# Performance work log

Measured on AMD Instinct MI355X. Metric: run time of the kernel, lower is better.

Reference implementation:

```python
import jax, jax.numpy as jnp
import numpy as np

B, L, H = 2, 2048, 1024
NH, DK, DV = 4, 256, 256
CONV_K, FIR_S, FIR_L = 4, 3, 63
GATE_IN = H + 4 * 2 * NH  # 1056
MLP_H = 2 * H
CHUNK = 32


def l2norm(x):
    return x * jax.lax.rsqrt(jnp.sum(x * x, -1, keepdims=True) + 1e-6)


def causal_dwconv(x, w):
    # x: [b, l, c], w: [c, k]; causal depthwise cross-correlation == F.conv1d(pad left k-1, groups=c)
    k = w.shape[-1]
    xc = jnp.pad(jnp.transpose(x, (0, 2, 1)), ((0, 0), (0, 0), (k - 1, 0)))
    y = jax.lax.conv_general_dilated(xc, w[:, None, :], (1,), 'VALID',
                                     feature_group_count=w.shape[0],
                                     dimension_numbers=('NCH', 'OIH', 'NCH'))
    return jnp.transpose(y, (0, 2, 1))


def delta_rule_chunkwise(q, k, v, beta, chunk=CHUNK):
    # q,k: [b,h,L,dk]; v: [b,h,L,dv]; beta: [b,h,L]; L divisible by chunk
    b, h, Lp, dk = q.shape
    dv = v.shape[-1]
    n = Lp // chunk
    q = l2norm(q)
    k = l2norm(k)
    v = v * beta[..., None]
    kb = k * beta[..., None]
    qc, kc, vc, kbc = (t.reshape(b, h, n, chunk, -1) for t in (q, k, v, kb))
    # strictly-lower Gram matrix; the original in-place row loop computes inv(I + tril(kb k^T, -1))
    A = jnp.tril(jnp.einsum('bhnid,bhnjd->bhnij', kbc, kc), -1)
    T = jnp.linalg.inv(jnp.eye(chunk, dtype=q.dtype) + A)  # [b,h,n,c,c]
    u = T @ vc   # [b,h,n,c,dv]
    w = T @ kbc  # [b,h,n,c,dk]

    def step(S, inp):
        qi, ki, ui, wi = inp  # each [b,h,c,d]
        attn = jnp.tril(qi @ jnp.swapaxes(ki, -1, -2))  # keep diag (masked_fill triu(.,1))
        u2 = ui - wi @ S
        oi = qi @ S + attn @ u2
        return S + jnp.swapaxes(ki, -1, -2) @ u2, oi

    S0 = jnp.zeros((b, h, dk, dv), q.dtype)
    xs = tuple(jnp.moveaxis(t, 2, 0) for t in (qc, kc, u, w))
    S, o = jax.lax.scan(step, S0, xs)
    o = jnp.moveaxis(o, 0, 2).reshape(b, h, Lp, dv)
    return o, S


def branch_stats(x):
    # x: [b,l,h,d] -> [b,l,2h]  (mean and population-std, std clamped at sqrt(1e-6))
    m = x.mean(-1)
    s = jnp.sqrt(jnp.maximum(x.var(-1), 1e-6))
    return jnp.concatenate([m, s], -1)


def setup_inputs() -> dict:
    key = jax.random.key(0)
    ks = jax.random.split(key, 16)
    f32 = jnp.float32

    def dirac(k_, shape):
        f = 0.01 * jax.random.normal(k_, shape, f32)
        return f.at[..., shape[-1] // 2].add(1.0)

    b2 = jnp.zeros((NH * 4,), f32).at[jnp.arange(NH) * 4 + 3].set(2.0)
    return {
        'hidden_states': jax.random.normal(ks[0], (B, L, H), f32),
        'Wq': 0.02 * jax.random.normal(ks[1], (H, NH * DK), f32),
        'Wk': 0.02 * jax.random.normal(ks[2], (H, NH * DK), f32),
        'Wv': 0.02 * jax.random.normal(ks[3], (H, NH * DV), f32),
        'Wb': 0.02 * jax.random.normal(ks[4], (H, NH), f32),
        'conv_q_w': 0.2 * jax.random.normal(ks[5], (NH * DK, CONV_K), f32),
        'conv_k_w': 0.2 * jax.random.normal(ks[6], (NH * DK, CONV_K), f32),
        'conv_v_w': 0.2 * jax.random.normal(ks[7], (NH * DV, CONV_K), f32),
        'fir_short_w': dirac(ks[8], (NH, DV, FIR_S)),
        'fir_long_w': dirac(ks[9], (NH, DV, FIR_L)),
        'mlp_w1': 0.02 * jax.random.normal(ks[10], (GATE_IN, MLP_H), f32),
        'mlp_b1': jnp.zeros((MLP_H,), f32),
        'mlp_w2': 0.02 * jax.random.normal(ks[11], (MLP_H, NH * 4), f32),
        'mlp_b2': b2,
        'gate_log_temp': jnp.full((NH,), np.log(1.2), f32),
        'o_norm_w': jnp.ones((DV,), f32),
        'Wo': 0.02 * jax.random.normal(ks[12], (NH * DV, H), f32),
    }


def reference(hidden_states, Wq, Wk, Wv, Wb, conv_q_w, conv_k_w, conv_v_w,
              fir_short_w, fir_long_w, mlp_w1, mlp_b1, mlp_w2, mlp_b2,
              gate_log_temp, o_norm_w, Wo):
    x = hidden_states
    b, l, _ = x.shape
    # projections + short causal depthwise convs with silu (qk_activation='silu')
    q = jax.nn.silu(causal_dwconv(x @ Wq, conv_q_w)).reshape(b, l, NH, DK)
    k = jax.nn.silu(causal_dwconv(x @ Wk, conv_k_w)).reshape(b, l, NH, DK)
    v = jax.nn.silu(causal_dwconv(x @ Wv, conv_v_w)).reshape(b, l, NH, DV)
    beta = jax.nn.sigmoid(x @ Wb)  # [b,l,h]

    delta_out, _S = delta_rule_chunkwise(
        jnp.transpose(q, (0, 2, 1, 3)), jnp.transpose(k, (0, 2, 1, 3)),
        jnp.transpose(v, (0, 2, 1, 3)), jnp.transpose(beta, (0, 2, 1)))
    delta_out = jnp.transpose(delta_out, (0, 2, 1, 3))  # [b,l,h,dv]

    vf = v.reshape(b, l, NH * DV)
    fir_short = causal_dwconv(vf, fir_short_w.reshape(NH * DV, FIR_S)).reshape(b, l, NH, DV)
    fir_long = causal_dwconv(vf, fir_long_w.reshape(NH * DV, FIR_L)).reshape(b, l, NH, DV)

    gate_in = jnp.concatenate([x, branch_stats(fir_short), branch_stats(fir_long),
                               branch_stats(delta_out), branch_stats(v)], -1)
    logits = jax.nn.gelu(gate_in @ mlp_w1 + mlp_b1, approximate=False) @ mlp_w2 + mlp_b2
    temp = jax.nn.softplus(gate_log_temp) + 1e-4
    logits = logits.reshape(b, l, NH, 4) / temp[None, None, :, None]
    w = jax.nn.softmax(logits, -1)

    o = (w[..., 0:1] * fir_short + w[..., 1:2] * fir_long
         + w[..., 2:3] * delta_out + w[..., 3:4] * v)
    # RMSNorm over head_v_dim, eps=1e-5
    o = o * jax.lax.rsqrt(jnp.mean(o * o, -1, keepdims=True) + 1e-5) * o_norm_w
    return o.reshape(b, l, NH * DV) @ Wo
```

## Files before the change

kernel.cpp:

```cpp
#include <hip/hip_runtime.h>
#include <hip/hip_bf16.h>


#define DEVI __device__ __forceinline__
typedef unsigned int u32;
typedef unsigned short ushort_t;
typedef __attribute__((ext_vector_type(8))) short short8;
typedef __attribute__((ext_vector_type(4))) float floatx4;

constexpr int Ls = 2048, NH = 4;
constexpr int NCh = 64;

constexpr size_t off_xq   = 0;
constexpr size_t off_xk   = 4194304;
constexpr size_t off_xv   = 8388608;
constexpr size_t off_q    = 12582912;
constexpr size_t off_k    = 16777216;
constexpr size_t off_v    = 20971520;
constexpr size_t off_beta = 25165824;
constexpr size_t off_attn = 25182208;
constexpr size_t off_firs = 25706496;
constexpr size_t off_firl = 29900800;
constexpr size_t off_gin  = 34095104;
constexpr size_t off_mlph = 38420480;
constexpr size_t off_gates= 46809088;

DEVI float sigmoidf_(float x) { return 1.f / (1.f + expf(-x)); }
DEVI float siluf_(float x) { return x / (1.f + expf(-x)); }
DEVI float geluf_(float x) { return 0.5f * x * (1.f + erff(x * 0.7071067811865476f)); }
DEVI ushort_t f2bf(float f) {
  union { float f; u32 u; } c{f};
  u32 r = (c.u + 0x7fffu + ((c.u >> 16) & 1u)) >> 16;
  return (ushort_t)r;
}
DEVI float bf2f(ushort_t h) {
  union { u32 u; float f; } c; c.u = ((u32)h) << 16; return c.f;
}
DEVI void cvt8(float4 a, float4 b, short8& hi, short8& lo) {
  float f[8] = {a.x,a.y,a.z,a.w,b.x,b.y,b.z,b.w};
#pragma unroll
  for (int j = 0; j < 8; ++j) {
    ushort_t h = f2bf(f[j]);
    hi[j] = (short)h;
    lo[j] = (short)f2bf(f[j] - bf2f(h));
  }
}
DEVI void async16(const void* g, void* l) {
  __builtin_amdgcn_global_load_lds(
      (const u32 __attribute__((address_space(1)))*)g,
      (u32 __attribute__((address_space(3)))*)l, 16, 0, 0);
}

__global__ __launch_bounds__(256) void to_bf16(
    const float* __restrict__ in, ushort_t* __restrict__ out, int n)
{
  int i = (blockIdx.x * 256 + threadIdx.x) * 8;
  if (i >= n) return;
  float4 a = *(const float4*)(in + i);
  float4 b = *(const float4*)(in + i + 4);
  ushort_t o[8] = { f2bf(a.x), f2bf(a.y), f2bf(a.z), f2bf(a.w),
                    f2bf(b.x), f2bf(b.y), f2bf(b.z), f2bf(b.w) };
  *(uint4*)(out + i) = *(uint4*)o;
}

__global__ __launch_bounds__(256) void convT(
    const float* __restrict__ W, ushort_t* __restrict__ out, int Kq, int Nq)
{
  __shared__ ushort_t tile[32][33];
  int n0 = blockIdx.x * 32, k0 = blockIdx.y * 32;
  int tx = threadIdx.x & 31, ty = threadIdx.x >> 5;
#pragma unroll
  for (int r = 0; r < 32; r += 8)
    tile[ty + r][tx] = f2bf(W[(size_t)(k0 + ty + r) * Nq + n0 + tx]);
  __syncthreads();
#pragma unroll
  for (int r = 0; r < 32; r += 8)
    out[(size_t)(n0 + ty + r) * Kq + k0 + tx] = tile[tx][ty + r];
}

__global__ __launch_bounds__(256) void gemm_bf16(
    const ushort_t* __restrict__ A, const ushort_t* __restrict__ Bt,
    float* __restrict__ C, int Nq, int Kq,
    const float* __restrict__ bias, int act, int outbf)
{
  __shared__ ushort_t As[128 * 32];
  __shared__ ushort_t Bs[128 * 32];
  int t = threadIdx.x;
  int w = t >> 6, lane = t & 63;
  int m0 = blockIdx.y * 128, n0 = blockIdx.x * 128;
  floatx4 acc[4][4];
#pragma unroll
  for (int i = 0; i < 4; ++i)
#pragma unroll
    for (int j = 0; j < 4; ++j)
#pragma unroll
      for (int r = 0; r < 4; ++r) acc[i][j][r] = 0.f;

  int lrow = lane >> 2, lk8 = (lane & 3) * 8;
  for (int kt = 0; kt < Kq; kt += 32) {
#pragma unroll
    for (int r = 0; r < 2; ++r) {
      int seg = w * 2 + r;
      int row = seg * 16 + lrow;
      async16(A  + (size_t)(m0 + row) * Kq + kt + lk8, &As[seg * 512]);
      async16(Bt + (size_t)(n0 + row) * Kq + kt + lk8, &Bs[seg * 512]);
    }
    __syncthreads();
    short8 af[4], bf[4];
#pragma unroll
    for (int i = 0; i < 4; ++i) {
      int row = (w >> 1) * 64 + i * 16 + (lane & 15);
      af[i] = *(const short8*)&As[row * 32 + (lane >> 4) * 8];
    }
#pragma unroll
    for (int j = 0; j < 4; ++j) {
      int col = (w & 1) * 64 + j * 16 + (lane & 15);
      bf[j] = *(const short8*)&Bs[col * 32 + (lane >> 4) * 8];
    }
#pragma unroll
    for (int i = 0; i < 4; ++i)
#pragma unroll
      for (int j = 0; j < 4; ++j)
        acc[i][j] = __builtin_amdgcn_mfma_f32_16x16x32_bf16(af[i], bf[j], acc[i][j], 0, 0, 0);
    __syncthreads();
  }
#pragma unroll
  for (int i = 0; i < 4; ++i) {
    int rbase = m0 + (w >> 1) * 64 + i * 16 + ((lane >> 4) << 2);
#pragma unroll
    for (int j = 0; j < 4; ++j) {
      int col = n0 + (w & 1) * 64 + j * 16 + (lane & 15);
      float bv = act ? bias[col] : 0.f;
#pragma unroll
      for (int r = 0; r < 4; ++r) {
        float v = acc[i][j][r];
        if (act) v = geluf_(v + bv);
        if (outbf) ((ushort_t*)C)[(size_t)(rbase + r) * Nq + col] = f2bf(v);
        else       C[(size_t)(rbase + r) * Nq + col] = v;
      }
    }
  }
}

__global__ __launch_bounds__(256) void beta_sigmoid(
    const float* __restrict__ x, const float* __restrict__ Wb,
    float* __restrict__ beta)
{
  int mtok = blockIdx.x, t = threadIdx.x;
  int b = mtok >> 11, l = mtok & 2047;
  float a0 = 0, a1 = 0, a2 = 0, a3 = 0;
  for (int k = t; k < 1024; k += 256) {
    float xv = x[(size_t)mtok * 1024 + k];
    float4 w4 = *(const float4*)(Wb + k * 4);
    a0 = fmaf(xv, w4.x, a0); a1 = fmaf(xv, w4.y, a1);
    a2 = fmaf(xv, w4.z, a2); a3 = fmaf(xv, w4.w, a3);
  }
#pragma unroll
  for (int off = 32; off; off >>= 1) {
    a0 += __shfl_down(a0, off); a1 += __shfl_down(a1, off);
    a2 += __shfl_down(a2, off); a3 += __shfl_down(a3, off);
  }
  __shared__ float red[4][4];
  int w = t >> 6;
  if ((t & 63) == 0) { red[w][0] = a0; red[w][1] = a1; red[w][2] = a2; red[w][3] = a3; }
  __syncthreads();
  if (t < 4) {
    float s = red[0][t] + red[1][t] + red[2][t] + red[3][t];
    beta[((size_t)(b * NH + t)) * Ls + l] = sigmoidf_(s);
  }
}

__global__ __launch_bounds__(256) void conv_prep(
    const float* __restrict__ x3, const float* __restrict__ wq,
    const float* __restrict__ wk, const float* __restrict__ wv,
    const float* __restrict__ beta_g,
    float* __restrict__ qn, float* __restrict__ kn,
    float* __restrict__ kb, float* __restrict__ vb,
    float* __restrict__ v_out)
{
  int i = blockIdx.x;
  int t = threadIdx.x;
  int l = i & 2047, bh = i >> 11;
  int b = bh >> 2, h = bh & 3;
  int c = h * 256 + t;
  const float* p = x3 + ((size_t)b * Ls) * 3072 + c;
  float4 wq4 = *(const float4*)(wq + c * 4);
  float4 wk4 = *(const float4*)(wk + c * 4);
  float4 wv4 = *(const float4*)(wv + c * 4);
  float qw[4] = {wq4.x, wq4.y, wq4.z, wq4.w};
  float kw[4] = {wk4.x, wk4.y, wk4.z, wk4.w};
  float vw[4] = {wv4.x, wv4.y, wv4.z, wv4.w};
  float aq = 0.f, ak = 0.f, av = 0.f;
#pragma unroll
  for (int j = 0; j < 4; ++j) {
    int ls = l - 3 + j;
    if (ls >= 0) {
      size_t rb = (size_t)ls * 3072;
      aq = fmaf(qw[j], p[rb], aq);
      ak = fmaf(kw[j], p[rb + 1024], ak);
      av = fmaf(vw[j], p[rb + 2048], av);
    }
  }
  float qv = siluf_(aq), kv = siluf_(ak), vv = siluf_(av);
  float sq = qv * qv, sk = kv * kv;
#pragma unroll
  for (int off = 32; off; off >>= 1) {
    sq += __shfl_down(sq, off);
    sk += __shfl_down(sk, off);
  }
  __shared__ float rq_[4], rk_[4];
  int w = t >> 6;
  if ((t & 63) == 0) { rq_[w] = sq; rk_[w] = sk; }
  __syncthreads();
  sq = rq_[0] + rq_[1] + rq_[2] + rq_[3];
  sk = rk_[0] + rk_[1] + rk_[2] + rk_[3];
  float rq = rsqrtf(sq + 1e-6f), rk = rsqrtf(sk + 1e-6f);
  float bt = beta_g[i];
  size_t base = (size_t)i * 256 + t;
  qn[base] = qv * rq;
  kn[base] = kv * rk;
  kb[base] = kv * rk * bt;
  vb[base] = vv * bt;
  v_out[base] = vv;
}

__global__ __launch_bounds__(256) void chunk_prep(
    const float* __restrict__ kb, const float* __restrict__ kn,
    const float* __restrict__ qn, const float* __restrict__ vb,
    float* __restrict__ attn_g, float* __restrict__ u_out,
    ushort_t* __restrict__ wn_bf, ushort_t* __restrict__ q_bf,
    ushort_t* __restrict__ knT_bf)
{
  __shared__ float Am[32][33];
  __shared__ float Tm[32][36];
  __shared__ ushort_t KT_hi[256][40];
  __shared__ ushort_t KT_lo[256][40];
  int t = threadIdx.x;
  int cc = blockIdx.x & 63, bh = blockIdx.x >> 6;
  size_t gbase = ((size_t)bh * Ls + cc * 32) * 256;
  int wv = t >> 6, lane = t & 63;
  int l16 = lane & 15, quad = lane >> 4;
  int mi = wv >> 1, ni = wv & 1;

  floatx4 Aacc = {0.f,0.f,0.f,0.f}, Qacc = {0.f,0.f,0.f,0.f};
  {
    int mrow = mi * 16 + l16, nrow = ni * 16 + l16;
    const float* kbp = kb + gbase + (size_t)mrow * 256;
    const float* qnp = qn + gbase + (size_t)mrow * 256;
    const float* knp = kn + gbase + (size_t)nrow * 256;
#pragma unroll
    for (int ks = 0; ks < 8; ++ks) {
      int koff = ks * 32 + quad * 8;
      short8 kbh, kbl, qnh, qnl, knh, knl;
      cvt8(*(const float4*)(kbp + koff), *(const float4*)(kbp + koff + 4), kbh, kbl);
      cvt8(*(const float4*)(qnp + koff), *(const float4*)(qnp + koff + 4), qnh, qnl);
      cvt8(*(const float4*)(knp + koff), *(const float4*)(knp + koff + 4), knh, knl);
      Aacc = __builtin_amdgcn_mfma_f32_16x16x32_bf16(kbh, knh, Aacc, 0, 0, 0);
      Aacc = __builtin_amdgcn_mfma_f32_16x16x32_bf16(kbh, knl, Aacc, 0, 0, 0);
      Aacc = __builtin_amdgcn_mfma_f32_16x16x32_bf16(kbl, knh, Aacc, 0, 0, 0);
      Qacc = __builtin_amdgcn_mfma_f32_16x16x32_bf16(qnh, knh, Qacc, 0, 0, 0);
      Qacc = __builtin_amdgcn_mfma_f32_16x16x32_bf16(qnh, knl, Qacc, 0, 0, 0);
      Qacc = __builtin_amdgcn_mfma_f32_16x16x32_bf16(qnl, knh, Qacc, 0, 0, 0);
      if (ni == 0)
        *(uint4*)(q_bf + gbase + (size_t)mrow * 256 + koff) = *(uint4*)&qnh;
    }
  }
  float* ag = attn_g + ((size_t)bh * 64 + cc) * 1024;
#pragma unroll
  for (int r = 0; r < 4; ++r) {
    int row = mi * 16 + quad * 4 + r, col = ni * 16 + l16;
    Am[row][col] = (col < row) ? Aacc[r] : 0.f;
    ag[row * 32 + col] = (col <= row) ? Qacc[r] : 0.f;
  }
  __syncthreads();

  if (wv == 0) {
    if (t < 32) {
#pragma unroll
      for (int i = 0; i < 32; ++i) Tm[i][t] = (i == t) ? 1.f : 0.f;
      for (int i2 = 1; i2 < 32; ++i2) {
        if (t < i2) {
          float s = 0.f;
          for (int m2 = t; m2 < i2; ++m2) s = fmaf(Am[i2][m2], Tm[m2][t], s);
          Tm[i2][t] = -s;
        }
      }
    }
  } else {
    int base = t - 64;
#pragma unroll
    for (int pass = 0; pass < 2; ++pass) {
      int d = base + pass * 192;
      if (d < 256) {
        u32 hp[16], lp[16], kp2[16];
#pragma unroll
        for (int m2 = 0; m2 < 16; ++m2) {
          float f0 = kb[gbase + (size_t)(2 * m2) * 256 + d];
          float f1 = kb[gbase + (size_t)(2 * m2 + 1) * 256 + d];
          ushort_t h0 = f2bf(f0), h1 = f2bf(f1);
          hp[m2] = (u32)h0 | ((u32)h1 << 16);
          lp[m2] = (u32)f2bf(f0 - bf2f(h0)) | ((u32)f2bf(f1 - bf2f(h1)) << 16);
          float g0 = kn[gbase + (size_t)(2 * m2) * 256 + d];
          float g1 = kn[gbase + (size_t)(2 * m2 + 1) * 256 + d];
          kp2[m2] = (u32)f2bf(g0) | ((u32)f2bf(g1) << 16);
        }
#pragma unroll
        for (int q2 = 0; q2 < 4; ++q2) {
          *(uint4*)&KT_hi[d][q2 * 8] = *(uint4*)&hp[q2 * 4];
          *(uint4*)&KT_lo[d][q2 * 8] = *(uint4*)&lp[q2 * 4];
          *(uint4*)(knT_bf + gbase + (size_t)d * 32 + q2 * 8) = *(uint4*)&kp2[q2 * 4];
        }
      }
    }
  }
  __syncthreads();

  int lt = wv & 1, dgrp = wv >> 1;
  short8 Th, Tl;
  {
    int lrow = lt * 16 + l16;
    cvt8(*(const float4*)&Tm[lrow][quad * 8],
         *(const float4*)&Tm[lrow][quad * 8 + 4], Th, Tl);
  }
#pragma unroll
  for (int j = 0; j < 8; ++j) {
    int dt = dgrp * 8 + j;
    short8 Bh = *(const short8*)&KT_hi[dt * 16 + l16][quad * 8];
    short8 Bl = *(const short8*)&KT_lo[dt * 16 + l16][quad * 8];
    floatx4 acc = {0.f,0.f,0.f,0.f};
    acc = __builtin_amdgcn_mfma_f32_16x16x32_bf16(Th, Bh, acc, 0, 0, 0);
    acc = __builtin_amdgcn_mfma_f32_16x16x32_bf16(Th, Bl, acc, 0, 0, 0);
    acc = __builtin_amdgcn_mfma_f32_16x16x32_bf16(Tl, Bh, acc, 0, 0, 0);
#pragma unroll
    for (int r = 0; r < 4; ++r) {
      int row = lt * 16 + quad * 4 + r;
      wn_bf[gbase + (size_t)row * 256 + dt * 16 + l16] = f2bf(-acc[r]);
    }
  }
  __syncthreads();

  {
    int d = t;
    u32 hp[16], lp[16];
#pragma unroll
    for (int m2 = 0; m2 < 16; ++m2) {
      float f0 = vb[gbase + (size_t)(2 * m2) * 256 + d];
      float f1 = vb[gbase + (size_t)(2 * m2 + 1) * 256 + d];
      ushort_t h0 = f2bf(f0), h1 = f2bf(f1);
      hp[m2] = (u32)h0 | ((u32)h1 << 16);
      lp[m2] = (u32)f2bf(f0 - bf2f(h0)) | ((u32)f2bf(f1 - bf2f(h1)) << 16);
    }
#pragma unroll
    for (int q2 = 0; q2 < 4; ++q2) {
      *(uint4*)&KT_hi[d][q2 * 8] = *(uint4*)&hp[q2 * 4];
      *(uint4*)&KT_lo[d][q2 * 8] = *(uint4*)&lp[q2 * 4];
    }
  }
  __syncthreads();

#pragma unroll
  for (int j = 0; j < 8; ++j) {
    int dt = dgrp * 8 + j;
    short8 Bh = *(const short8*)&KT_hi[dt * 16 + l16][quad * 8];
    short8 Bl = *(const short8*)&KT_lo[dt * 16 + l16][quad * 8];
    floatx4 acc = {0.f,0.f,0.f,0.f};
    acc = __builtin_amdgcn_mfma_f32_16x16x32_bf16(Th, Bh, acc, 0, 0, 0);
    acc = __builtin_amdgcn_mfma_f32_16x16x32_bf16(Th, Bl, acc, 0, 0, 0);
    acc = __builtin_amdgcn_mfma_f32_16x16x32_bf16(Tl, Bh, acc, 0, 0, 0);
#pragma unroll
    for (int r = 0; r < 4; ++r) {
      int row = lt * 16 + quad * 4 + r;
      u_out[gbase + (size_t)row * 256 + dt * 16 + l16] = acc[r];
    }
  }
}

__global__ __launch_bounds__(256, 1) void delta_fir(
    const ushort_t* __restrict__ wn_bf, const ushort_t* __restrict__ q_bf,
    const ushort_t* __restrict__ knT_bf, const float* __restrict__ attn_g,
    const float* __restrict__ u_g, float* __restrict__ delta_g,
    const float* __restrict__ v, const float* __restrict__ wlg,
    const float* __restrict__ wsg, float* __restrict__ firl,
    float* __restrict__ firs)
{
  __shared__ __attribute__((aligned(16))) char smem[72704];
  int t = threadIdx.x;

  if (blockIdx.x >= 128) {
    float (*vt)[71] = (float(*)[71])smem;
    int bid = blockIdx.x - 128;
    int lt = bid & 255;
    int bh = bid >> 8;
    int b = bh >> 2, h = bh & 3;
    int l0 = lt * 8;
    const float* vp = v + (size_t)bh * Ls * 256;
    for (int r = 0; r < 70; ++r) {
      int ls = l0 - 62 + r;
      vt[t][r] = (ls >= 0) ? vp[(size_t)ls * 256 + t] : 0.f;
    }
    float TL[63], TS3[3];
#pragma unroll
    for (int j = 0; j < 63; ++j) TL[j] = wlg[((size_t)h * 256 + t) * 63 + j];
#pragma unroll
    for (int j = 0; j < 3; ++j) TS3[j] = wsg[((size_t)h * 256 + t) * 3 + j];
    __syncthreads();
    float aL[8] = {0,0,0,0,0,0,0,0}, aS[8] = {0,0,0,0,0,0,0,0};
#pragma unroll
    for (int r = 0; r < 70; ++r) {
      float vm = vt[t][r];
#pragma unroll
      for (int p = 0; p < 8; ++p) {
        int jl = r - p;
        if (jl >= 0 && jl < 63) aL[p] = fmaf(vm, TL[jl], aL[p]);
        int jssrc = r - 60 - p;
        if (jssrc >= 0 && jssrc < 3) aS[p] = fmaf(vm, TS3[jssrc], aS[p]);
      }
    }
#pragma unroll
    for (int p = 0; p < 8; ++p) {
      int l = l0 + p;
      size_t ob = (((size_t)b * Ls + l) * NH + h) * 256 + t;
      firl[ob] = aL[p];
      firs[ob] = aS[p];
    }
    return;
  }

  ushort_t (*Shi)[264] = (ushort_t(*)[264])(smem);
  ushort_t (*Slo)[264] = (ushort_t(*)[264])(smem + 8448);
  float (*u2L)[17] = (float(*)[17])(smem + 16896);
  int bh = blockIdx.x & 7, g = blockIdx.x >> 3;
  int b = bh >> 2, h = bh & 3;
  int wv = t >> 6, lane = t & 63;
  int lquad = lane >> 4, l16 = lane & 15;
  int j0 = g * 16;
  const ushort_t* wp = wn_bf + (size_t)bh * Ls * 256;
  const ushort_t* qp = q_bf  + (size_t)bh * Ls * 256;
  const ushort_t* kp = knT_bf + (size_t)bh * Ls * 256;
  const float* up = u_g + (size_t)bh * Ls * 256;
  const float* atp = attn_g + (size_t)bh * 64 * 1024;
  int Mt = wv & 1;
  bool isU = (wv < 2);
  floatx4 Sacc[4], SaccL[4];
#pragma unroll
  for (int i = 0; i < 4; ++i)
#pragma unroll
    for (int r = 0; r < 4; ++r) { Sacc[i][r] = 0.f; SaccL[i][r] = 0.f; }
  for (int i = t; i < 4224; i += 256) ((u32*)smem)[i] = 0;
  __syncthreads();
  const ushort_t* ap = (isU ? wp : qp) + (size_t)(Mt * 16 + l16) * 256;
  const ushort_t* kr = kp + (size_t)l16 * 32 + lquad * 8;
  const float* urow = up + (size_t)(Mt * 16 + lquad * 4) * 256 + j0 + l16;
  const float* arp = atp + (size_t)(Mt * 16 + l16) * 32 + lquad * 8;

  short8 aC[8], kC[4];
  floatx4 uC = {0.f, 0.f, 0.f, 0.f};
  float4 atC0 = {0,0,0,0}, atC1 = {0,0,0,0};
#pragma unroll
  for (int ks = 0; ks < 8; ++ks)
    aC[ks] = *(const short8*)(ap + ks * 32 + lquad * 8);
#pragma unroll
  for (int i = 0; i < 4; ++i)
    kC[i] = *(const short8*)(kr + (size_t)(wv * 4 + i) * 512);
  if (isU) {
#pragma unroll
    for (int r = 0; r < 4; ++r) uC[r] = urow[(size_t)r * 256];
  } else {
    atC0 = *(const float4*)(arp);
    atC1 = *(const float4*)(arp + 4);
  }

  for (int cc = 0; cc < NCh; ++cc) {
    size_t cb = (size_t)cc * 8192;
    short8 aN[8], kN[4];
    floatx4 uN = {0.f, 0.f, 0.f, 0.f};
    float4 atN0 = {0,0,0,0}, atN1 = {0,0,0,0};
    bool hasN = (cc + 1 < NCh);
    if (hasN) {
      size_t nb = cb + 8192;
#pragma unroll
      for (int ks = 0; ks < 8; ++ks)
        aN[ks] = *(const short8*)(ap + nb + ks * 32 + lquad * 8);
#pragma unroll
      for (int i = 0; i < 4; ++i)
        kN[i] = *(const short8*)(kr + nb + (size_t)(wv * 4 + i) * 512);
      if (isU) {
#pragma unroll
        for (int r = 0; r < 4; ++r) uN[r] = urow[nb + (size_t)r * 256];
      } else {
        size_t na = (size_t)(cc + 1) * 1024;
        atN0 = *(const float4*)(arp + na);
        atN1 = *(const float4*)(arp + na + 4);
      }
    }
    short8 ath, atl;
    if (!isU) cvt8(atC0, atC1, ath, atl);

    floatx4 acc;
    if (isU) {
      floatx4 a0 = uC, a1 = {0,0,0,0}, a2 = {0,0,0,0}, a3 = {0,0,0,0};
#pragma unroll
      for (int ks = 0; ks < 8; ++ks) {
        short8 sh = *(const short8*)&Shi[l16][ks * 32 + lquad * 8];
        short8 sl = *(const short8*)&Slo[l16][ks * 32 + lquad * 8];
        if (ks & 1) {
          a1 = __builtin_amdgcn_mfma_f32_16x16x32_bf16(aC[ks], sh, a1, 0, 0, 0);
          a3 = __builtin_amdgcn_mfma_f32_16x16x32_bf16(aC[ks], sl, a3, 0, 0, 0);
        } else {
          a0 = __builtin_amdgcn_mfma_f32_16x16x32_bf16(aC[ks], sh, a0, 0, 0, 0);
          a2 = __builtin_amdgcn_mfma_f32_16x16x32_bf16(aC[ks], sl, a2, 0, 0, 0);
        }
      }
#pragma unroll
      for (int r = 0; r < 4; ++r) acc[r] = (a0[r] + a1[r]) + (a2[r] + a3[r]);
#pragma unroll
      for (int r = 0; r < 4; ++r)
        u2L[Mt * 16 + lquad * 4 + r][l16] = acc[r];
    } else {
      floatx4 a0 = {0,0,0,0}, a1 = {0,0,0,0};
#pragma unroll
      for (int ks = 0; ks < 8; ++ks) {
        short8 sh = *(const short8*)&Shi[l16][ks * 32 + lquad * 8];
        if (ks & 1) a1 = __builtin_amdgcn_mfma_f32_16x16x32_bf16(aC[ks], sh, a1, 0, 0, 0);
        else        a0 = __builtin_amdgcn_mfma_f32_16x16x32_bf16(aC[ks], sh, a0, 0, 0, 0);
      }
#pragma unroll
      for (int r = 0; r < 4; ++r) acc[r] = a0[r] + a1[r];
    }
    __syncthreads();
    short8 uh, ul;
#pragma unroll
    for (int j = 0; j < 8; ++j) {
      float f = u2L[lquad * 8 + j][l16];
      ushort_t hi = f2bf(f);
      uh[j] = (short)hi;
      ul[j] = (short)f2bf(f - bf2f(hi));
    }
    if (!isU) {
      acc = __builtin_amdgcn_mfma_f32_16x16x32_bf16(ath, uh, acc, 0, 0, 0);
      acc = __builtin_amdgcn_mfma_f32_16x16x32_bf16(ath, ul, acc, 0, 0, 0);
      acc = __builtin_amdgcn_mfma_f32_16x16x32_bf16(atl, uh, acc, 0, 0, 0);
#pragma unroll
      for (int r = 0; r < 4; ++r) {
        int l = cc * 32 + Mt * 16 + lquad * 4 + r;
        delta_g[(((size_t)b * Ls + l) * NH + h) * 256 + j0 + l16] = acc[r];
      }
    }
#pragma unroll
    for (int i = 0; i < 4; ++i) {
      Sacc[i]  = __builtin_amdgcn_mfma_f32_16x16x32_bf16(kC[i], uh, Sacc[i], 0, 0, 0);
      SaccL[i] = __builtin_amdgcn_mfma_f32_16x16x32_bf16(kC[i], ul, SaccL[i], 0, 0, 0);
    }
#pragma unroll
    for (int i = 0; i < 4; ++i) {
      int dk0 = (wv * 4 + i) * 16 + lquad * 4;
      ushort4 h4, l4;
      ushort_t* hp = (ushort_t*)&h4;
      ushort_t* lp = (ushort_t*)&l4;
#pragma unroll
      for (int r = 0; r < 4; ++r) {
        float sv = Sacc[i][r] + SaccL[i][r];
        ushort_t hi = f2bf(sv);
        hp[r] = hi;
        lp[r] = f2bf(sv - bf2f(hi));
      }
      *(ushort4*)&Shi[l16][dk0] = h4;
      *(ushort4*)&Slo[l16][dk0] = l4;
    }
    __syncthreads();
    if (hasN) {
#pragma unroll
      for (int ks = 0; ks < 8; ++ks) aC[ks] = aN[ks];
#pragma unroll
      for (int i = 0; i < 4; ++i) kC[i] = kN[i];
      uC = uN;
      atC0 = atN0; atC1 = atN1;
    }
  }
}

__global__ __launch_bounds__(256) void build_gate_in_bf(
    const float* __restrict__ x, const float* __restrict__ firs,
    const float* __restrict__ firl, const float* __restrict__ delta,
    const float* __restrict__ v, ushort_t* __restrict__ gin)
{
  int mtok = blockIdx.x, t = threadIdx.x;
  int b = mtok >> 11, l = mtok & 2047;
  float4 xv = *(const float4*)(x + (size_t)mtok * 1024 + t * 4);
  ushort4 xo = make_ushort4(f2bf(xv.x), f2bf(xv.y), f2bf(xv.z), f2bf(xv.w));
  *(ushort4*)(gin + (size_t)mtok * 1056 + t * 4) = xo;
  int w = t >> 6, lane = t & 63;
  for (int br = 0; br < 4; ++br) {
    float s = 0.f, s2 = 0.f;
#pragma unroll
    for (int r = 0; r < 4; ++r) {
      int d = lane + r * 64;
      float val;
      if (br == 0)      val = firs [(size_t)mtok * 1024 + w * 256 + d];
      else if (br == 1) val = firl [(size_t)mtok * 1024 + w * 256 + d];
      else if (br == 2) val = delta[(size_t)mtok * 1024 + w * 256 + d];
      else              val = v[(((size_t)(b * NH + w)) * Ls + l) * 256 + d];
      s += val; s2 = fmaf(val, val, s2);
    }
#pragma unroll
    for (int off = 32; off; off >>= 1) {
      s += __shfl_down(s, off);
      s2 += __shfl_down(s2, off);
    }
    if (lane == 0) {
      float mean = s * (1.f / 256.f);
      float var = s2 * (1.f / 256.f) - mean * mean;
      gin[(size_t)mtok * 1056 + 1024 + br * 8 + w] = f2bf(mean);
      gin[(size_t)mtok * 1056 + 1024 + br * 8 + 4 + w] = f2bf(sqrtf(fmaxf(var, 1e-6f)));
    }
  }
}

__global__ __launch_bounds__(256) void mlp2_gates(
    const ushort_t* __restrict__ mh, const float* __restrict__ W2,
    const float* __restrict__ b2, const float* __restrict__ glt,
    float* __restrict__ gates)
{
  int mtok = blockIdx.x, t = threadIdx.x;
  float p[16];
#pragma unroll
  for (int j = 0; j < 16; ++j) p[j] = 0.f;
  for (int k = t; k < 2048; k += 256) {
    float hv = bf2f(mh[(size_t)mtok * 2048 + k]);
    const float* wr = W2 + (size_t)k * 16;
#pragma unroll
    for (int j4 = 0; j4 < 4; ++j4) {
      float4 w4 = *(const float4*)(wr + j4 * 4);
      p[j4*4+0] = fmaf(hv, w4.x, p[j4*4+0]);
      p[j4*4+1] = fmaf(hv, w4.y, p[j4*4+1]);
      p[j4*4+2] = fmaf(hv, w4.z, p[j4*4+2]);
      p[j4*4+3] = fmaf(hv, w4.w, p[j4*4+3]);
    }
  }
#pragma unroll
  for (int j = 0; j < 16; ++j)
#pragma unroll
    for (int off = 32; off; off >>= 1) p[j] += __shfl_down(p[j], off);
  __shared__ float red[4][16];
  __shared__ float zl[16];
  int w = t >> 6;
  if ((t & 63) == 0) {
#pragma unroll
    for (int j = 0; j < 16; ++j) red[w][j] = p[j];
  }
  __syncthreads();
  if (t < 16) {
    float tot = red[0][t] + red[1][t] + red[2][t] + red[3][t] + b2[t];
    float tempv = log1pf(expf(glt[t >> 2])) + 1e-4f;
    zl[t] = tot / tempv;
  }
  __syncthreads();
  if (t < 4) {
    float z0 = zl[t*4], z1 = zl[t*4+1], z2 = zl[t*4+2], z3 = zl[t*4+3];
    float mx = fmaxf(fmaxf(z0, z1), fmaxf(z2, z3));
    float e0 = expf(z0 - mx), e1 = expf(z1 - mx), e2 = expf(z2 - mx), e3 = expf(z3 - mx);
    float inv = 1.f / (e0 + e1 + e2 + e3);
    gates[(size_t)mtok * 16 + t * 4 + 0] = e0 * inv;
    gates[(size_t)mtok * 16 + t * 4 + 1] = e1 * inv;
    gates[(size_t)mtok * 16 + t * 4 + 2] = e2 * inv;
    gates[(size_t)mtok * 16 + t * 4 + 3] = e3 * inv;
  }
}

__global__ __launch_bounds__(256) void combine_norm_bf(
    const float* __restrict__ firs, const float* __restrict__ firl,
    const float* __restrict__ delta, const float* __restrict__ v,
    const float* __restrict__ gates, const float* __restrict__ onw,
    ushort_t* __restrict__ o)
{
  int mh = blockIdx.x;
  int mtok = mh >> 2, h = mh & 3;
  int t = threadIdx.x;
  int b = mtok >> 11, l = mtok & 2047;
  const float* g = gates + (size_t)mtok * 16 + h * 4;
  float w0 = g[0], w1 = g[1], w2 = g[2], w3 = g[3];
  size_t tb = (size_t)mtok * 1024 + h * 256 + t;
  float val = w0 * firs[tb] + w1 * firl[tb] + w2 * delta[tb]
            + w3 * v[(((size_t)(b * NH + h)) * Ls + l) * 256 + t];
  float s2 = val * val;
#pragma unroll
  for (int off = 32; off; off >>= 1) s2 += __shfl_down(s2, off);
  __shared__ float r4[4];
  if ((t & 63) == 0) r4[t >> 6] = s2;
  __syncthreads();
  float tot = r4[0] + r4[1] + r4[2] + r4[3];
  float rms = rsqrtf(tot * (1.f / 256.f) + 1e-5f);
  o[tb] = f2bf(val * rms * onw[t]);
}

extern "C" void kernel_launch(void* const* d_in, const int* in_sizes, int n_in,
                              void* d_out, int out_size, void* d_ws, size_t ws_size,
                              hipStream_t stream) {
  const float* x     = (const float*)d_in[0];
  const float* Wq    = (const float*)d_in[1];
  const float* Wk    = (const float*)d_in[2];
  const float* Wv    = (const float*)d_in[3];
  const float* Wb    = (const float*)d_in[4];
  const float* convq = (const float*)d_in[5];
  const float* convk = (const float*)d_in[6];
  const float* convv = (const float*)d_in[7];
  const float* firsw = (const float*)d_in[8];
  const float* firlw = (const float*)d_in[9];
  const float* mlpw1 = (const float*)d_in[10];
  const float* mlpb1 = (const float*)d_in[11];
  const float* mlpw2 = (const float*)d_in[12];
  const float* mlpb2 = (const float*)d_in[13];
  const float* glt   = (const float*)d_in[14];
  const float* onw   = (const float*)d_in[15];
  const float* Wo    = (const float*)d_in[16];
  float* ws = (float*)d_ws;

  ushort_t* x_bf   = (ushort_t*)(ws + off_firs);
  ushort_t* Wqkv_t = (ushort_t*)(ws + off_firl);
  ushort_t* gin_bf = (ushort_t*)(ws + off_gin);
  ushort_t* w1_t   = (ushort_t*)(ws + off_k);
  ushort_t* o_bf   = (ushort_t*)(ws + off_xv);
  ushort_t* Wo_t   = (ushort_t*)(ws + off_beta);
  ushort_t* mlph_bf= (ushort_t*)(ws + off_mlph);
  ushort_t* wn_bf  = (ushort_t*)(ws + off_firs);
  ushort_t* q_bf   = (ushort_t*)(ws + off_firs + 2097152);
  ushort_t* knT_bf = (ushort_t*)(ws + off_firl);
  float* x3   = ws + off_xq;
  float* kb_f = ws + off_gin;
  float* vb_f = ws + off_mlph;
  float* firs_f = ws + off_xq;
  float* firl_f = ws + off_xk;

  dim3 blk(256);
  to_bf16<<<2048, blk, 0, stream>>>(x, x_bf, 4194304);
  convT<<<dim3(32, 32), blk, 0, stream>>>(Wq, Wqkv_t, 1024, 1024);
  convT<<<dim3(32, 32), blk, 0, stream>>>(Wk, Wqkv_t + 1048576, 1024, 1024);
  convT<<<dim3(32, 32), blk, 0, stream>>>(Wv, Wqkv_t + 2097152, 1024, 1024);
  gemm_bf16<<<dim3(24, 32), blk, 0, stream>>>(x_bf, Wqkv_t, x3, 3072, 1024, nullptr, 0, 0);
  beta_sigmoid<<<4096, blk, 0, stream>>>(x, Wb, ws + off_beta);
  conv_prep<<<16384, blk, 0, stream>>>(x3, convq, convk, convv, ws + off_beta,
                                       ws + off_q, ws + off_k, kb_f, vb_f, ws + off_v);
  chunk_prep<<<512, blk, 0, stream>>>(kb_f, ws + off_k, ws + off_q, vb_f,
                                      ws + off_attn, ws + off_xv, wn_bf, q_bf, knT_bf);
  delta_fir<<<2176, blk, 0, stream>>>(wn_bf, q_bf, knT_bf, ws + off_attn,
                                      ws + off_xv, ws + off_q,
                                      ws + off_v, firlw, firsw, firl_f, firs_f);
  build_gate_in_bf<<<4096, blk, 0, stream>>>(x, firs_f, firl_f, ws + off_q,
                                             ws + off_v, gin_bf);
  convT<<<dim3(64, 33), blk, 0, stream>>>(mlpw1, w1_t, 1056, 2048);
  gemm_bf16<<<dim3(16, 32), blk, 0, stream>>>(gin_bf, w1_t, (float*)mlph_bf,
                                              2048, 1056, mlpb1, 1, 1);
  mlp2_gates<<<4096, blk, 0, stream>>>(mlph_bf, mlpw2, mlpb2, glt, ws + off_gates);
  combine_norm_bf<<<16384, blk, 0, stream>>>(firs_f, firl_f, ws + off_q,
                                             ws + off_v, ws + off_gates, onw, o_bf);
  convT<<<dim3(32, 32), blk, 0, stream>>>(Wo, Wo_t, 1024, 1024);
  gemm_bf16<<<dim3(8, 32), blk, 0, stream>>>(o_bf, Wo_t, (float*)d_out, 1024, 1024, nullptr, 0, 0);
}
```

Baseline: 581.9 us.

## Process chunk pairs in delta recurrence using precomputed cross-chunk products

Adds a cross_prep kernel that precomputes, for each pair of adjacent chunks, W1·K0ᵀ and Q1·K0ᵀ. The sequential delta scan can then handle two chunks per iteration: the second chunk's u2 and output are corrected with these precomputed terms rather than waiting for the state to be updated after the first chunk. Full __syncthreads are replaced by a lighter LDS-wait plus s_barrier, and the u2 staging buffer is doubled. This is meant to shorten the serial dependency chain and cut barriers per chunk, at the cost of an extra kernel, extra memory traffic, and bf16-only precision on the cross term inputs (kn stored as hi only).

```diff
diff --git a/kernel.cpp b/kernel.cpp
--- a/kernel.cpp
+++ b/kernel.cpp
@@ -9,7 +9,6 @@
 typedef __attribute__((ext_vector_type(4))) float floatx4;
 
 constexpr int Ls = 2048, NH = 4;
-constexpr int NCh = 64;
 
 constexpr size_t off_xq   = 0;
 constexpr size_t off_xk   = 4194304;
@@ -50,6 +49,12 @@
       (const u32 __attribute__((address_space(1)))*)g,
       (u32 __attribute__((address_space(3)))*)l, 16, 0, 0);
 }
+DEVI void wave_barrier() {
+  __builtin_amdgcn_sched_barrier(0);
+  asm volatile("s_waitcnt lgkmcnt(0)" ::: "memory");
+  __builtin_amdgcn_s_barrier();
+  __builtin_amdgcn_sched_barrier(0);
+}
 
 __global__ __launch_bounds__(256) void to_bf16(
     const float* __restrict__ in, ushort_t* __restrict__ out, int n)
@@ -229,7 +234,7 @@
     const float* __restrict__ qn, const float* __restrict__ vb,
     float* __restrict__ attn_g, float* __restrict__ u_out,
     ushort_t* __restrict__ wn_bf, ushort_t* __restrict__ q_bf,
-    ushort_t* __restrict__ knT_bf)
+    ushort_t* __restrict__ knT_bf, ushort_t* __restrict__ kn_bf)
 {
   __shared__ float Am[32][33];
   __shared__ float Tm[32][36];
@@ -263,6 +268,8 @@
       Qacc = __builtin_amdgcn_mfma_f32_16x16x32_bf16(qnl, knh, Qacc, 0, 0, 0);
       if (ni == 0)
         *(uint4*)(q_bf + gbase + (size_t)mrow * 256 + koff) = *(uint4*)&qnh;
+      if (mi == 0)
+        *(uint4*)(kn_bf + gbase + (size_t)nrow * 256 + koff) = *(uint4*)&knh;
     }
   }
   float* ag = attn_g + ((size_t)bh * 64 + cc) * 1024;
@@ -375,10 +382,44 @@
   }
 }
 
+__global__ __launch_bounds__(256) void cross_prep(
+    const ushort_t* __restrict__ wn_bf, const ushort_t* __restrict__ q_bf,
+    const ushort_t* __restrict__ kn_bf,
+    float* __restrict__ X_g, float* __restrict__ Y_g)
+{
+  int t = threadIdx.x;
+  int sc = blockIdx.x & 31, bh = blockIdx.x >> 5;
+  int wv = t >> 6, lane = t & 63;
+  int l16 = lane & 15, quad = lane >> 4;
+  int mi = wv >> 1, ni = wv & 1;
+  size_t base = (size_t)bh * Ls * 256;
+  size_t r1 = base + (size_t)(sc * 64 + 32 + mi * 16 + l16) * 256;
+  size_t r0 = base + (size_t)(sc * 64 + ni * 16 + l16) * 256;
+  floatx4 Xacc = {0.f,0.f,0.f,0.f}, Yacc = {0.f,0.f,0.f,0.f};
+#pragma unroll
+  for (int ks = 0; ks < 8; ++ks) {
+    int ko = ks * 32 + quad * 8;
+    short8 aw = *(const short8*)(wn_bf + r1 + ko);
+    short8 aq = *(const short8*)(q_bf  + r1 + ko);
+    short8 bk = *(const short8*)(kn_bf + r0 + ko);
+    Xacc = __builtin_amdgcn_mfma_f32_16x16x32_bf16(aw, bk, Xacc, 0, 0, 0);
+    Yacc = __builtin_amdgcn_mfma_f32_16x16x32_bf16(aq, bk, Yacc, 0, 0, 0);
+  }
+  float* xo = X_g + ((size_t)bh * 32 + sc) * 1024;
+  float* yo = Y_g + ((size_t)bh * 32 + sc) * 1024;
+#pragma unroll
+  for (int r = 0; r < 4; ++r) {
+    int row = mi * 16 + quad * 4 + r, col = ni * 16 + l16;
+    xo[row * 32 + col] = Xacc[r];
+    yo[row * 32 + col] = Yacc[r];
+  }
+}
+
 __global__ __launch_bounds__(256, 1) void delta_fir(
     const ushort_t* __restrict__ wn_bf, const ushort_t* __restrict__ q_bf,
     const ushort_t* __restrict__ knT_bf, const float* __restrict__ attn_g,
-    const float* __restrict__ u_g, float* __restrict__ delta_g,
+    const float* __restrict__ u_g, const float* __restrict__ X_g,
+    const float* __restrict__ Y_g, float* __restrict__ delta_g,
     const float* __restrict__ v, const float* __restrict__ wlg,
     const float* __restrict__ wsg, float* __restrict__ firl,
     float* __restrict__ firs)
@@ -428,128 +469,219 @@
 
   ushort_t (*Shi)[264] = (ushort_t(*)[264])(smem);
   ushort_t (*Slo)[264] = (ushort_t(*)[264])(smem + 8448);
-  float (*u2L)[17] = (float(*)[17])(smem + 16896);
+  float (*u2L0)[17] = (float(*)[17])(smem + 16896);
+  float (*u2L1)[17] = (float(*)[17])(smem + 19072);
   int bh = blockIdx.x & 7, g = blockIdx.x >> 3;
   int b = bh >> 2, h = bh & 3;
   int wv = t >> 6, lane = t & 63;
   int lquad = lane >> 4, l16 = lane & 15;
   int j0 = g * 16;
+  int Mt = wv & 1;
+  bool isU = (wv < 2);
   const ushort_t* wp = wn_bf + (size_t)bh * Ls * 256;
   const ushort_t* qp = q_bf  + (size_t)bh * Ls * 256;
-  const ushort_t* kp = knT_bf + (size_t)bh * Ls * 256;
-  const float* up = u_g + (size_t)bh * Ls * 256;
-  const float* atp = attn_g + (size_t)bh * 64 * 1024;
-  int Mt = wv & 1;
-  bool isU = (wv < 2);
+  const ushort_t* ap = (isU ? wp : qp) + (size_t)(Mt * 16 + l16) * 256;
+  const ushort_t* kr = knT_bf + (size_t)bh * Ls * 256 + (size_t)l16 * 32 + lquad * 8;
+  const float* urow = u_g + (size_t)bh * Ls * 256
+                    + (size_t)(Mt * 16 + lquad * 4) * 256 + j0 + l16;
+  const float* arp = attn_g + (size_t)bh * 64 * 1024
+                   + (size_t)(Mt * 16 + l16) * 32 + lquad * 8;
+  const float* xrp = (isU ? X_g : Y_g) + (size_t)bh * 32768
+                   + (size_t)(Mt * 16 + l16) * 32 + lquad * 8;
+
   floatx4 Sacc[4], SaccL[4];
 #pragma unroll
   for (int i = 0; i < 4; ++i)
 #pragma unroll
     for (int r = 0; r < 4; ++r) { Sacc[i][r] = 0.f; SaccL[i][r] = 0.f; }
   for (int i = t; i < 4224; i += 256) ((u32*)smem)[i] = 0;
-  __syncthreads();
-  const ushort_t* ap = (isU ? wp : qp) + (size_t)(Mt * 16 + l16) * 256;
-  const ushort_t* kr = kp + (size_t)l16 * 32 + lquad * 8;
-  const float* urow = up + (size_t)(Mt * 16 + lquad * 4) * 256 + j0 + l16;
-  const float* arp = atp + (size_t)(Mt * 16 + l16) * 32 + lquad * 8;
-
-  short8 aC[8], kC[4];
-  floatx4 uC = {0.f, 0.f, 0.f, 0.f};
-  float4 atC0 = {0,0,0,0}, atC1 = {0,0,0,0};
+
+  short8 a0[8], k0[4];
+  floatx4 u0 = {0.f, 0.f, 0.f, 0.f};
+  float4 at0a = {0,0,0,0}, at0b = {0,0,0,0};
 #pragma unroll
   for (int ks = 0; ks < 8; ++ks)
-    aC[ks] = *(const short8*)(ap + ks * 32 + lquad * 8);
+    a0[ks] = *(const short8*)(ap + ks * 32 + lquad * 8);
 #pragma unroll
   for (int i = 0; i < 4; ++i)
-    kC[i] = *(const short8*)(kr + (size_t)(wv * 4 + i) * 512);
+    k0[i] = *(const short8*)(kr + (size_t)(wv * 4 + i) * 512);
   if (isU) {
 #pragma unroll
-    for (int r = 0; r < 4; ++r) uC[r] = urow[(size_t)r * 256];
+    for (int r = 0; r < 4; ++r) u0[r] = urow[(size_t)r * 256];
   } else {
-    atC0 = *(const float4*)(arp);
-    atC1 = *(const float4*)(arp + 4);
-  }
-
-  for (int cc = 0; cc < NCh; ++cc) {
-    size_t cb = (size_t)cc * 8192;
-    short8 aN[8], kN[4];
-    floatx4 uN = {0.f, 0.f, 0.f, 0.f};
-    float4 atN0 = {0,0,0,0}, atN1 = {0,0,0,0};
-    bool hasN = (cc + 1 < NCh);
-    if (hasN) {
-      size_t nb = cb + 8192;
-#pragma unroll
-      for (int ks = 0; ks < 8; ++ks)
-        aN[ks] = *(const short8*)(ap + nb + ks * 32 + lquad * 8);
-#pragma unroll
-      for (int i = 0; i < 4; ++i)
-        kN[i] = *(const short8*)(kr + nb + (size_t)(wv * 4 + i) * 512);
-      if (isU) {
-#pragma unroll
-        for (int r = 0; r < 4; ++r) uN[r] = urow[nb + (size_t)r * 256];
-      } else {
-        size_t na = (size_t)(cc + 1) * 1024;
-        atN0 = *(const float4*)(arp + na);
-        atN1 = *(const float4*)(arp + na + 4);
-      }
-    }
-    short8 ath, atl;
-    if (!isU) cvt8(atC0, atC1, ath, atl);
-
-    floatx4 acc;
+    at0a = *(const float4*)(arp);
+    at0b = *(const float4*)(arp + 4);
+  }
+  wave_barrier();
+
+  for (int sc = 0; sc < 32; ++sc) {
+    size_t cb1 = (size_t)sc * 16384 + 8192;
+    size_t nb0 = (size_t)(sc + 1) * 16384;
+    bool hasN = (sc + 1 < 32);
+
+    short8 a1[8], k1[4];
+    floatx4 u1 = {0.f, 0.f, 0.f, 0.f};
+    float4 at1a = {0,0,0,0}, at1b = {0,0,0,0};
+#pragma unroll
+    for (int ks = 0; ks < 8; ++ks)
+      a1[ks] = *(const short8*)(ap + cb1 + ks * 32 + lquad * 8);
+#pragma unroll
+    for (int i = 0; i < 4; ++i)
+      k1[i] = *(const short8*)(kr + cb1 + (size_t)(wv * 4 + i) * 512);
     if (isU) {
-      floatx4 a0 = uC, a1 = {0,0,0,0}, a2 = {0,0,0,0}, a3 = {0,0,0,0};
+#pragma unroll
+      for (int r = 0; r < 4; ++r) u1[r] = urow[cb1 + (size_t)r * 256];
+    } else {
+      size_t na = (size_t)(2 * sc + 1) * 1024;
+      at1a = *(const float4*)(arp + na);
+      at1b = *(const float4*)(arp + na + 4);
+    }
+    float4 xa = *(const float4*)(xrp + (size_t)sc * 1024);
+    float4 xb = *(const float4*)(xrp + (size_t)sc * 1024 + 4);
+
+    floatx4 acc0;
+    if (isU) {
+      floatx4 A0 = u0, A1 = {0,0,0,0}, A2 = {0,0,0,0}, A3 = {0,0,0,0};
 #pragma unroll
       for (int ks = 0; ks < 8; ++ks) {
         short8 sh = *(const short8*)&Shi[l16][ks * 32 + lquad * 8];
         short8 sl = *(const short8*)&Slo[l16][ks * 32 + lquad * 8];
         if (ks & 1) {
-          a1 = __builtin_amdgcn_mfma_f32_16x16x32_bf16(aC[ks], sh, a1, 0, 0, 0);
-          a3 = __builtin_amdgcn_mfma_f32_16x16x32_bf16(aC[ks], sl, a3, 0, 0, 0);
+          A1 = __builtin_amdgcn_mfma_f32_16x16x32_bf16(a0[ks], sh, A1, 0, 0, 0);
+          A3 = __builtin_amdgcn_mfma_f32_16x16x32_bf16(a0[ks], sl, A3, 0, 0, 0);
         } else {
-          a0 = __builtin_amdgcn_mfma_f32_16x16x32_bf16(aC[ks], sh, a0, 0, 0, 0);
-          a2 = __builtin_amdgcn_mfma_f32_16x16x32_bf16(aC[ks], sl, a2, 0, 0, 0);
+          A0 = __builtin_amdgcn_mfma_f32_16x16x32_bf16(a0[ks], sh, A0, 0, 0, 0);
+          A2 = __builtin_amdgcn_mfma_f32_16x16x32_bf16(a0[ks], sl, A2, 0, 0, 0);
         }
       }
 #pragma unroll
-      for (int r = 0; r < 4; ++r) acc[r] = (a0[r] + a1[r]) + (a2[r] + a3[r]);
+      for (int r = 0; r < 4; ++r) acc0[r] = (A0[r] + A1[r]) + (A2[r] + A3[r]);
 #pragma unroll
       for (int r = 0; r < 4; ++r)
-        u2L[Mt * 16 + lquad * 4 + r][l16] = acc[r];
+        u2L0[Mt * 16 + lquad * 4 + r][l16] = acc0[r];
     } else {
-      floatx4 a0 = {0,0,0,0}, a1 = {0,0,0,0};
+      floatx4 A0 = {0,0,0,0}, A1 = {0,0,0,0};
 #pragma unroll
       for (int ks = 0; ks < 8; ++ks) {
         short8 sh = *(const short8*)&Shi[l16][ks * 32 + lquad * 8];
-        if (ks & 1) a1 = __builtin_amdgcn_mfma_f32_16x16x32_bf16(aC[ks], sh, a1, 0, 0, 0);
-        else        a0 = __builtin_amdgcn_mfma_f32_16x16x32_bf16(aC[ks], sh, a0, 0, 0, 0);
-      }
-#pragma unroll
-      for (int r = 0; r < 4; ++r) acc[r] = a0[r] + a1[r];
-    }
-    __syncthreads();
-    short8 uh, ul;
+        if (ks & 1) A1 = __builtin_amdgcn_mfma_f32_16x16x32_bf16(a0[ks], sh, A1, 0, 0, 0);
+        else        A0 = __builtin_amdgcn_mfma_f32_16x16x32_bf16(a0[ks], sh, A0, 0, 0, 0);
+      }
+#pragma unroll
+      for (int r = 0; r < 4; ++r) acc0[r] = A0[r] + A1[r];
+    }
+    if (hasN) {
+#pragma unroll
+      for (int ks = 0; ks < 8; ++ks)
+        a0[ks] = *(const short8*)(ap + nb0 + ks * 32 + lquad * 8);
+    }
+    wave_barrier();
+
+    short8 uh0, ul0;
 #pragma unroll
     for (int j = 0; j < 8; ++j) {
-      float f = u2L[lquad * 8 + j][l16];
+      float f = u2L0[lquad * 8 + j][l16];
       ushort_t hi = f2bf(f);
-      uh[j] = (short)hi;
-      ul[j] = (short)f2bf(f - bf2f(hi));
+      uh0[j] = (short)hi;
+      ul0[j] = (short)f2bf(f - bf2f(hi));
+    }
+#pragma unroll
+    for (int i = 0; i < 4; ++i) {
+      Sacc[i]  = __builtin_amdgcn_mfma_f32_16x16x32_bf16(k0[i], uh0, Sacc[i], 0, 0, 0);
+      SaccL[i] = __builtin_amdgcn_mfma_f32_16x16x32_bf16(k0[i], ul0, SaccL[i], 0, 0, 0);
+    }
+    if (hasN) {
+#pragma unroll
+      for (int i = 0; i < 4; ++i)
+        k0[i] = *(const short8*)(kr + nb0 + (size_t)(wv * 4 + i) * 512);
+    }
+
+    floatx4 acc1;
+    if (isU) {
+      floatx4 A0 = u1, A1 = {0,0,0,0}, A2 = {0,0,0,0}, A3 = {0,0,0,0};
+#pragma unroll
+      for (int ks = 0; ks < 8; ++ks) {
+        short8 sh = *(const short8*)&Shi[l16][ks * 32 + lquad * 8];
+        short8 sl = *(const short8*)&Slo[l16][ks * 32 + lquad * 8];
+        if (ks & 1) {
+          A1 = __builtin_amdgcn_mfma_f32_16x16x32_bf16(a1[ks], sh, A1, 0, 0, 0);
+          A3 = __builtin_amdgcn_mfma_f32_16x16x32_bf16(a1[ks], sl, A3, 0, 0, 0);
+        } else {
+          A0 = __builtin_amdgcn_mfma_f32_16x16x32_bf16(a1[ks], sh, A0, 0, 0, 0);
+          A2 = __builtin_amdgcn_mfma_f32_16x16x32_bf16(a1[ks], sl, A2, 0, 0, 0);
+        }
+      }
+      short8 Xh, Xl;
+      cvt8(xa, xb, Xh, Xl);
+      A0 = __builtin_amdgcn_mfma_f32_16x16x32_bf16(Xh, uh0, A0, 0, 0, 0);
+      A1 = __builtin_amdgcn_mfma_f32_16x16x32_bf16(Xh, ul0, A1, 0, 0, 0);
+      A2 = __builtin_amdgcn_mfma_f32_16x16x32_bf16(Xl, uh0, A2, 0, 0, 0);
+#pragma unroll
+      for (int r = 0; r < 4; ++r) acc1[r] = (A0[r] + A1[r]) + (A2[r] + A3[r]);
+#pragma unroll
+      for (int r = 0; r < 4; ++r)
+        u2L1[Mt * 16 + lquad * 4 + r][l16] = acc1[r];
+      if (hasN) {
+#pragma unroll
+        for (int r = 0; r < 4; ++r) u0[r] = urow[nb0 + (size_t)r * 256];
+      }
+    } else {
+      short8 ath, atl;
+      cvt8(at0a, at0b, ath, atl);
+      acc0 = __builtin_amdgcn_mfma_f32_16x16x32_bf16(ath, uh0, acc0, 0, 0, 0);
+      acc0 = __builtin_amdgcn_mfma_f32_16x16x32_bf16(ath, ul0, acc0, 0, 0, 0);
+      acc0 = __builtin_amdgcn_mfma_f32_16x16x32_bf16(atl, uh0, acc0, 0, 0, 0);
+#pragma unroll
+      for (int r = 0; r < 4; ++r) {
+        int l = sc * 64 + Mt * 16 + lquad * 4 + r;
+        delta_g[(((size_t)b * Ls + l) * NH + h) * 256 + j0 + l16] = acc0[r];
+      }
+      floatx4 A0 = {0,0,0,0}, A1 = {0,0,0,0};
+#pragma unroll
+      for (int ks = 0; ks < 8; ++ks) {
+        short8 sh = *(const short8*)&Shi[l16][ks * 32 + lquad * 8];
+        if (ks & 1) A1 = __builtin_amdgcn_mfma_f32_16x16x32_bf16(a1[ks], sh, A1, 0, 0, 0);
+        else        A0 = __builtin_amdgcn_mfma_f32_16x16x32_bf16(a1[ks], sh, A0, 0, 0, 0);
+      }
+      short8 Yh, Yl;
+      cvt8(xa, xb, Yh, Yl);
+      A0 = __builtin_amdgcn_mfma_f32_16x16x32_bf16(Yh, uh0, A0, 0, 0, 0);
+      A1 = __builtin_amdgcn_mfma_f32_16x16x32_bf16(Yh, ul0, A1, 0, 0, 0);
+      A0 = __builtin_amdgcn_mfma_f32_16x16x32_bf16(Yl, uh0, A0, 0, 0, 0);
+#pragma unroll
+      for (int r = 0; r < 4; ++r) acc1[r] = A0[r] + A1[r];
+      if (hasN) {
+        size_t na0 = (size_t)(2 * sc + 2) * 1024;
+        at0a = *(const float4*)(arp + na0);
+        at0b = *(const float4*)(arp + na0 + 4);
+      }
+    }
+    wave_barrier();
+
+    short8 uh1, ul1;
+#pragma unroll
+    for (int j = 0; j < 8; ++j) {
+      float f = u2L1[lquad * 8 + j][l16];
+      ushort_t hi = f2bf(f);
+      uh1[j] = (short)hi;
+      ul1[j] = (short)f2bf(f - bf2f(hi));
+    }
+#pragma unroll
+    for (int i = 0; i < 4; ++i) {
+      Sacc[i]  = __builtin_amdgcn_mfma_f32_16x16x32_bf16(k1[i], uh1, Sacc[i], 0, 0, 0);
+      SaccL[i] = __builtin_amdgcn_mfma_f32_16x16x32_bf16(k1[i], ul1, SaccL[i], 0, 0, 0);
     }
     if (!isU) {
-      acc = __builtin_amdgcn_mfma_f32_16x16x32_bf16(ath, uh, acc, 0, 0, 0);
-      acc = __builtin_amdgcn_mfma_f32_16x16x32_bf16(ath, ul, acc, 0, 0, 0);
-      acc = __builtin_amdgcn_mfma_f32_16x16x32_bf16(atl, uh, acc, 0, 0, 0);
+      short8 ath, atl;
+      cvt8(at1a, at1b, ath, atl);
+      acc1 = __builtin_amdgcn_mfma_f32_16x16x32_bf16(ath, uh1, acc1, 0, 0, 0);
+      acc1 = __builtin_amdgcn_mfma_f32_16x16x32_bf16(ath, ul1, acc1, 0, 0, 0);
+      acc1 = __builtin_amdgcn_mfma_f32_16x16x32_bf16(atl, uh1, acc1, 0, 0, 0);
 #pragma unroll
       for (int r = 0; r < 4; ++r) {
-        int l = cc * 32 + Mt * 16 + lquad * 4 + r;
-        delta_g[(((size_t)b * Ls + l) * NH + h) * 256 + j0 + l16] = acc[r];
-      }
-    }
-#pragma unroll
-    for (int i = 0; i < 4; ++i) {
-      Sacc[i]  = __builtin_amdgcn_mfma_f32_16x16x32_bf16(kC[i], uh, Sacc[i], 0, 0, 0);
-      SaccL[i] = __builtin_amdgcn_mfma_f32_16x16x32_bf16(kC[i], ul, SaccL[i], 0, 0, 0);
+        int l = sc * 64 + 32 + Mt * 16 + lquad * 4 + r;
+        delta_g[(((size_t)b * Ls + l) * NH + h) * 256 + j0 + l16] = acc1[r];
+      }
     }
 #pragma unroll
     for (int i = 0; i < 4; ++i) {
@@ -567,15 +699,7 @@
       *(ushort4*)&Shi[l16][dk0] = h4;
       *(ushort4*)&Slo[l16][dk0] = l4;
     }
-    __syncthreads();
-    if (hasN) {
-#pragma unroll
-      for (int ks = 0; ks < 8; ++ks) aC[ks] = aN[ks];
-#pragma unroll
-      for (int i = 0; i < 4; ++i) kC[i] = kN[i];
-      uC = uN;
-      atC0 = atN0; atC1 = atN1;
-    }
+    wave_barrier();
   }
 }
 
@@ -725,9 +849,12 @@
   ushort_t* wn_bf  = (ushort_t*)(ws + off_firs);
   ushort_t* q_bf   = (ushort_t*)(ws + off_firs + 2097152);
   ushort_t* knT_bf = (ushort_t*)(ws + off_firl);
+  ushort_t* kn_bf  = (ushort_t*)(ws + off_xq);
   float* x3   = ws + off_xq;
   float* kb_f = ws + off_gin;
   float* vb_f = ws + off_mlph;
+  float* X_g  = ws + off_gin;
+  float* Y_g  = ws + off_gin + 262144;
   float* firs_f = ws + off_xq;
   float* firl_f = ws + off_xk;
 
@@ -741,9 +868,11 @@
   conv_prep<<<16384, blk, 0, stream>>>(x3, convq, convk, convv, ws + off_beta,
                                        ws + off_q, ws + off_k, kb_f, vb_f, ws + off_v);
   chunk_prep<<<512, blk, 0, stream>>>(kb_f, ws + off_k, ws + off_q, vb_f,
-                                      ws + off_attn, ws + off_xv, wn_bf, q_bf, knT_bf);
+                                      ws + off_attn, ws + off_xv, wn_bf, q_bf,
+                                      knT_bf, kn_bf);
+  cross_prep<<<256, blk, 0, stream>>>(wn_bf, q_bf, kn_bf, X_g, Y_g);
   delta_fir<<<2176, blk, 0, stream>>>(wn_bf, q_bf, knT_bf, ws + off_attn,
-                                      ws + off_xv, ws + off_q,
+                                      ws + off_xv, X_g, Y_g, ws + off_q,
                                       ws + off_v, firlw, firsw, firl_f, firs_f);
   build_gate_in_bf<<<4096, blk, 0, stream>>>(x, firs_f, firl_f, ws + off_q,
                                              ws + off_v, gin_bf);
```

After: 545.6 us. 6.2% less time.
